# Kernel optimization log

Hardware: AMD Instinct MI355X
Metric: run time of the kernel (lower is better)

The kernel has to match this reference:

```python
import jax, jax.numpy as jnp
import numpy as np

D = 512      # embeddings_dim (in_features == out_features)
H = 4        # num_heads
MID = 2048   # mid_features
B, S = 4, 2048
EPS = 1e-5


def _ln(x, g, b):
    mu = jnp.mean(x, axis=-1, keepdims=True)
    var = jnp.mean(jnp.square(x - mu), axis=-1, keepdims=True)
    return g * (x - mu) / jnp.sqrt(var + EPS) + b


def setup_inputs() -> dict:
    key = jax.random.key(0)
    ks = jax.random.split(key, 16)
    w = 0.02  # weight init scale
    return {
        "x_encoder": jax.random.normal(ks[0], (B, S, D), jnp.float32),
        "x_decoder": jax.random.normal(ks[1], (B, S, D), jnp.float32),
        # per-head full-width projections (each head is a D->D Linear)
        "Wq": jax.random.normal(ks[2], (H, D, D), jnp.float32) * w,
        "bq": jnp.zeros((H, D), jnp.float32),
        "Wk": jax.random.normal(ks[3], (H, D, D), jnp.float32) * w,
        "bk": jnp.zeros((H, D), jnp.float32),
        "Wv": jax.random.normal(ks[4], (H, D, D), jnp.float32) * w,
        "bv": jnp.zeros((H, D), jnp.float32),
        # out_reshaper: Rearrange('b h s d -> b s (d h)') then Linear(D*H -> D)
        "Wo": jax.random.normal(ks[5], (D * H, D), jnp.float32) * w,
        "bo": jnp.zeros((D,), jnp.float32),
        "ln1_g": jnp.ones((D,), jnp.float32), "ln1_b": jnp.zeros((D,), jnp.float32),
        "ln2_g": jnp.ones((D,), jnp.float32), "ln2_b": jnp.zeros((D,), jnp.float32),
        # FouriFeedForward: D -> MID -> D with SELU
        "W1": jax.random.normal(ks[6], (D, MID), jnp.float32) * w,
        "b1": jnp.zeros((MID,), jnp.float32),
        "W2": jax.random.normal(ks[7], (MID, D), jnp.float32) * w,
        "b2": jnp.zeros((D,), jnp.float32),
        "ln3_g": jnp.ones((D,), jnp.float32), "ln3_b": jnp.zeros((D,), jnp.float32),
    }


def reference(x_encoder, x_decoder, Wq, bq, Wk, bk, Wv, bv, Wo, bo,
              ln1_g, ln1_b, ln2_g, ln2_b, W1, b1, W2, b2, ln3_g, ln3_b):
    # Fourier token mixing: per-batch fftn over (seq, feature) dims, keep real part
    xf = jnp.fft.fftn(x_decoder, axes=(1, 2)).real
    xd = _ln(x_decoder + xf, ln1_g, ln1_b)  # [B,S,D]

    # Linear multi-head attention: q from decoder, k/v from encoder.
    # qs/ks/vs: [B,H,S,D]; softmax over the HEAD axis (dim=1 in torch)
    qs = jax.nn.softmax(jnp.einsum('bsd,hde->bhse', xd, Wq) + bq[None, :, None, :], axis=1)
    ks = jax.nn.softmax(jnp.einsum('bsd,hde->bhse', x_encoder, Wk) + bk[None, :, None, :], axis=1)
    vs = jnp.einsum('bsd,hde->bhse', x_encoder, Wv) + bv[None, :, None, :]

    gc = jnp.einsum('bhsd,bhse->bhde', ks, vs)       # [B,H,D,D] global contexts
    out = jnp.einsum('bhsd,bhde->bhse', qs, gc)      # [B,H,S,D]

    # Rearrange 'b h s d -> b s (d h)': d is the slow axis, h the fast axis
    b, h, s, d = out.shape
    out = out.transpose(0, 2, 3, 1).reshape(b, s, d * h)
    attn = out @ Wo + bo                              # [B,S,D]

    x = _ln(xd + attn, ln2_g, ln2_b)
    ff = jax.nn.selu(x @ W1 + b1) @ W2 + b2           # dropout_p=0 (eval)
    x = _ln(x + ff, ln3_g, ln3_b)
    return x
```

## Files before the change

### kernel.cpp

```cpp
#include <hip/hip_runtime.h>
#include <stdint.h>

typedef __bf16 bf16;
typedef __bf16 bf16x8 __attribute__((ext_vector_type(8)));
typedef float f32x4 __attribute__((ext_vector_type(4)));

static __device__ __forceinline__ void async16(const void* g, void* l) {
  __builtin_amdgcn_global_load_lds(
      (__attribute__((address_space(1))) void*)g,
      (__attribute__((address_space(3))) void*)l, 16, 0, 0);
}

__global__ void __launch_bounds__(256) prep_all(
    const float* __restrict__ xdec, const float* __restrict__ xenc,
    bf16* __restrict__ Ttrig, bf16* __restrict__ Atrig2,
    bf16* __restrict__ xdec_b, bf16* __restrict__ xenc_b,
    const float* __restrict__ Wq, const float* __restrict__ Wk,
    const float* __restrict__ Wv, const float* __restrict__ Wo,
    const float* __restrict__ W1, const float* __restrict__ W2,
    bf16* __restrict__ BtQ, bf16* __restrict__ BtK, bf16* __restrict__ BtV,
    bf16* __restrict__ WoTh, bf16* __restrict__ W1T, bf16* __restrict__ W2T) {
  __shared__ bf16 tile[32][33];
  int id = blockIdx.x;
  if (id < 2048) {
    int idx = id * 256 + threadIdx.x;
    int d = idx & 511, jp = idx >> 9;
    int jj = jp >> 1, p = jp & 1;
    int t = (d * jj) & 511;
    float ang = (float)t * (6.283185307179586f / 512.0f);
    Ttrig[idx] = (bf16)(p ? __sinf(ang) : __cosf(ang));
  } else if (id < 11840) {
    int idx = (id - 2048) * 256 + threadIdx.x;
    int k = idx % 1088;
    int rr = idx / 1088;
    int r = rr % 1152, half = rr / 1152;
    float v = 0.0f;
    int tt = (r * k) & 2047;
    float ang = (float)tt * (6.283185307179586f / 2048.0f);
    if (half == 0) { if (r <= 1024 && k <= 1024) v = __cosf(ang); }
    else           { if (r <= 1023 && k >= 1 && k <= 1023) v = -__sinf(ang); }
    Atrig2[idx] = (bf16)v;
  } else if (id < 28224) {
    int i = (id - 11840) * 256 + threadIdx.x;
    xdec_b[i] = (bf16)xdec[i];
  } else if (id < 44608) {
    int i = (id - 28224) * 256 + threadIdx.x;
    xenc_b[i] = (bf16)xenc[i];
  } else {
    int id2 = id - 44608;
    int kind = id2 >> 10, t = id2 & 1023;
    const float* in; bf16* out; int R, C, rt, ct;
    bool iperm = false, qperm = false, hsel = false; int hh = 0;
    if (kind == 0)      { in = Wq; out = BtQ; R = 2048; C = 512; rt = t >> 4; ct = t & 15; iperm = true; qperm = true; }
    else if (kind == 1) { in = Wk; out = BtK; R = 2048; C = 512; rt = t >> 4; ct = t & 15; iperm = true; }
    else if (kind == 2) { in = Wv; out = BtV; R = 2048; C = 512; rt = t >> 4; ct = t & 15; iperm = true; }
    else if (kind == 3) {
      int zz = t >> 8, tt = t & 255;
      in = Wo; out = WoTh + (long)zz * 262144;
      R = 512; C = 512; rt = tt >> 4; ct = tt & 15; hsel = true; hh = zz;
    }
    else if (kind == 4) { in = W1; out = W1T; R = 512; C = 2048; rt = t >> 6; ct = t & 63; }
    else                { in = W2; out = W2T; R = 2048; C = 512; rt = t >> 4; ct = t & 15; }
    int c0 = ct * 32, r0 = rt * 32;
    int tx = threadIdx.x & 31, ty = threadIdx.x >> 5;
#pragma unroll
    for (int i = 0; i < 32; i += 8) {
      int r = r0 + ty + i;
      int rr = hsel ? (4 * r + hh) : r;
      tile[ty + i][tx] = (bf16)in[(long)rr * C + (c0 + tx)];
    }
    __syncthreads();
#pragma unroll
    for (int i = 0; i < 32; i += 8) {
      int cc = c0 + ty + i, rr = r0 + tx;
      if (iperm) {
        int e = cc, h = rr >> 9;
        int n = qperm ? ((e & 15) | (h << 4) | ((e >> 4) << 6)) : (4 * e + h);
        out[((long)n << 9) + (rr & 511)] = tile[tx][ty + i];
      } else {
        out[(long)cc * R + rr] = tile[tx][ty + i];
      }
    }
  }
}

__global__ void __launch_bounds__(256) fold_y(const bf16* __restrict__ Yt,
                                              bf16* __restrict__ Yf2) {
  int idx = blockIdx.x * 256 + threadIdx.x;
  int k = idx % 1088;
  int rr = idx / 1088;
  int j = rr & 511, z = rr >> 9;
  int b = z & 3, half = z >> 2;
  const bf16* yin = Yt + (long)b * 2097152 + (long)j * 4096;
  float v = 0.0f;
  if (half == 0) {
    if (k == 0) v = (float)yin[0];
    else if (k == 1024) v = (float)yin[1024];
    else if (k < 1024) v = (float)yin[k] + (float)yin[2048 - k];
  } else {
    if (k >= 1 && k <= 1023) v = (float)yin[2048 + k] - (float)yin[4096 - k];
  }
  Yf2[(long)z * 557056 + (long)j * 1088 + k] = (bf16)v;
}

__global__ void __launch_bounds__(256) ln1_kernel(
    const float* __restrict__ xdec, const bf16* __restrict__ CSb,
    const float* __restrict__ g, const float* __restrict__ be,
    bf16* __restrict__ outb) {
  const int row = blockIdx.x, t = threadIdx.x;
  const int b = row >> 11, s = row & 2047;
  const int sp = (s <= 1024) ? s : 2048 - s;
  const float sgn = (s <= 1024) ? 1.0f : -1.0f;
  const bf16* Crow = CSb + ((long)b * 1152 + sp) * 512;
  const bf16* Srow = CSb + ((long)(b + 4) * 1152 + sp) * 512;
  const long base = (long)row * 512;
  float v0 = xdec[base + t] + (float)Crow[t] + sgn * (float)Srow[t];
  float v1 = xdec[base + t + 256] + (float)Crow[t + 256] + sgn * (float)Srow[t + 256];
  float sm = v0 + v1, q = v0 * v0 + v1 * v1;
#pragma unroll
  for (int off = 32; off > 0; off >>= 1) {
    sm += __shfl_down(sm, off);
    q += __shfl_down(q, off);
  }
  __shared__ float red[8];
  const int wv = t >> 6, ln = t & 63;
  if (ln == 0) { red[wv] = sm; red[wv + 4] = q; }
  __syncthreads();
  float S = red[0] + red[1] + red[2] + red[3];
  float Q = red[4] + red[5] + red[6] + red[7];
  float mu = S * (1.0f / 512.0f);
  float var = Q * (1.0f / 512.0f) - mu * mu;
  float rstd = rsqrtf(var + 1e-5f);
  outb[base + t] = (bf16)(g[t] * (v0 - mu) * rstd + be[t]);
  outb[base + t + 256] = (bf16)(g[t + 256] * (v1 - mu) * rstd + be[t + 256]);
}

static __device__ __forceinline__ void smkv_body(
    int bid, bf16* lds,
    const bf16* __restrict__ klog, bf16* __restrict__ ksT,
    const bf16* __restrict__ vlog, bf16* __restrict__ vsT) {
  const int t = threadIdx.x;
  const bool isK = bid < 1024;
  int tb = isK ? bid : (bid - 1024);
  const bf16* src = isK ? klog : vlog;
  bf16* dst = isK ? ksT : vsT;
  int b = tb >> 8, rem = tb & 255;
  int s0 = (rem >> 3) << 6, e0 = (rem & 7) << 6;
  int te = t & 63, tr = t >> 6;
#pragma unroll
  for (int i = 0; i < 16; ++i) {
    int s = tr + (i << 2);
    bf16 raw[4] __attribute__((aligned(8)));
    *(uint2*)raw = *(const uint2*)(src + ((long)(b * 2048 + s0 + s) * 2048 + 4 * (e0 + te)));
    float x0 = (float)raw[0], x1 = (float)raw[1], x2 = (float)raw[2], x3 = (float)raw[3];
    if (isK) {
      float m = fmaxf(fmaxf(x0, x1), fmaxf(x2, x3));
      float y0 = __expf(x0 - m), y1 = __expf(x1 - m), y2 = __expf(x2 - m), y3 = __expf(x3 - m);
      float rs = 1.0f / (y0 + y1 + y2 + y3);
      x0 = y0 * rs; x1 = y1 * rs; x2 = y2 * rs; x3 = y3 * rs;
    }
    int cp = ((((s >> 2) ^ (te & 15)) << 2) | (s & 3));
    int base = te * 64 + cp;
    lds[base] = (bf16)x0;
    lds[4096 + base] = (bf16)x1;
    lds[8192 + base] = (bf16)x2;
    lds[12288 + base] = (bf16)x3;
  }
  __syncthreads();
  int sc = t & 15, r = t >> 4;
#pragma unroll
  for (int i = 0; i < 16; ++i) {
    int he = r + (i << 4);
    int h = he >> 6, e = he & 63;
    int cp = (sc ^ (e & 15)) << 2;
    bf16 tmp[4] __attribute__((aligned(8)));
    *(uint2*)tmp = *(const uint2*)&lds[h * 4096 + e * 64 + cp];
    *(uint2*)(dst + ((long)(b * 4 + h) * 512 + e0 + e) * 2048 + s0 + (sc << 2)) =
        *(const uint2*)tmp;
  }
}

template <typename TA, typename TB, int WRITE_BF16, int WRITE_F32>
__global__ void __launch_bounds__(256) ln_kernel(
    const TA* __restrict__ A, const TB* __restrict__ Bv,
    const float* __restrict__ g, const float* __restrict__ be,
    bf16* __restrict__ outb, float* __restrict__ outf) {
  const int row = blockIdx.x, t = threadIdx.x;
  const long base = (long)row * 512;
  float v0 = (float)A[base + t] + (float)Bv[base + t];
  float v1 = (float)A[base + t + 256] + (float)Bv[base + t + 256];
  float s = v0 + v1, q = v0 * v0 + v1 * v1;
#pragma unroll
  for (int off = 32; off > 0; off >>= 1) {
    s += __shfl_down(s, off);
    q += __shfl_down(q, off);
  }
  __shared__ float red[8];
  const int wv = t >> 6, ln = t & 63;
  if (ln == 0) { red[wv] = s; red[wv + 4] = q; }
  __syncthreads();
  float S = red[0] + red[1] + red[2] + red[3];
  float Q = red[4] + red[5] + red[6] + red[7];
  float mu = S * (1.0f / 512.0f);
  float var = Q * (1.0f / 512.0f) - mu * mu;
  float rstd = rsqrtf(var + 1e-5f);
  float o0 = g[t] * (v0 - mu) * rstd + be[t];
  float o1 = g[t + 256] * (v1 - mu) * rstd + be[t + 256];
  if (WRITE_BF16) { outb[base + t] = (bf16)o0; outb[base + t + 256] = (bf16)o1; }
  if (WRITE_F32)  { outf[base + t] = o0; outf[base + t + 256] = o1; }
}

template <int BN, int ADDR_MODE, int HAS_BIAS, int DO_SELU, int F32OUT, int SWIZ,
          int AHEAD>
static __device__ __forceinline__ void gemm_bt_body(
    int id, bf16* lA, bf16* lB,
    const bf16* __restrict__ A, const bf16* __restrict__ Bt,
    const float* __restrict__ bias, void* __restrict__ Cout,
    int N, int K, long sAz, long sBz, long sBiasz, long sCz,
    int gx, int gy, int gin) {
  int x, y, z;
  {
    if (SWIZ == 0) {
      x = id % gx; int t2 = id / gx; y = t2 % gy; z = t2 / gy;
    } else {
      int xcd = id & 7, r = id >> 3;
      int inner = r % gin, G = xcd + 8 * (r / gin);
      if (SWIZ == 1)      { y = G; x = inner % gx; z = inner / gx; }
      else if (SWIZ == 2) { z = G; x = inner % gx; y = inner / gx; }
      else                { x = G; y = inner % gy; z = inner / gy; }
    }
  }
  A  += (AHEAD == 1) ? sAz * (z & 3) : (AHEAD == 2) ? sAz * (z >> 2) : sAz * z;
  Bt += sBz * z;
  const int m0 = y * 128, n0 = x * BN;
  const int t = threadIdx.x;
  const int lane = t & 63, wave = t >> 6;
  const int srow = t >> 3;
  const int pch  = t & 7;
  const int lch  = pch ^ (srow & 7);
  const bf16* Ag = A  + (long)(m0 + srow) * K + lch * 8;
  const bf16* Bg = Bt + (long)(n0 + srow) * K + lch * 8;
  bf16* lAp = lA + srow * 64 + pch * 8;
  bf16* lBp = lB + srow * 64 + pch * 8;
  constexpr int MI = (BN == 128) ? 4 : 2;
  const int wm = (BN == 128) ? (wave >> 1) * 64 : wave * 32;
  const int wn = (BN == 128) ? (wave & 1) * 64 : 0;
  const int fr = lane & 15, fq = lane >> 4;

  f32x4 acc[MI][4] = {};

  for (int k0 = 0; k0 < K; k0 += 64) {
    __syncthreads();
#pragma unroll
    for (int i = 0; i < 4; ++i)
      async16(Ag + k0 + (long)(32 * i) * K, lAp + 32 * i * 64);
#pragma unroll
    for (int i = 0; i < BN / 32; ++i)
      async16(Bg + k0 + (long)(32 * i) * K, lBp + 32 * i * 64);
    __syncthreads();
#pragma unroll
    for (int kk = 0; kk < 2; ++kk) {
      bf16x8 av[MI], bfrag[4];
#pragma unroll
      for (int mi = 0; mi < MI; ++mi) {
        int r = wm + mi * 16 + fr;
        int c = (kk * 4 + fq) ^ (r & 7);
        av[mi] = *(const bf16x8*)&lA[r * 64 + c * 8];
      }
#pragma unroll
      for (int ni = 0; ni < 4; ++ni) {
        int r = wn + ni * 16 + fr;
        int c = (kk * 4 + fq) ^ (r & 7);
        bfrag[ni] = *(const bf16x8*)&lB[r * 64 + c * 8];
      }
#pragma unroll
      for (int mi = 0; mi < MI; ++mi)
#pragma unroll
        for (int ni = 0; ni < 4; ++ni)
          acc[mi][ni] = __builtin_amdgcn_mfma_f32_16x16x32_bf16(
              av[mi], bfrag[ni], acc[mi][ni], 0, 0, 0);
    }
  }

#pragma unroll
  for (int mi = 0; mi < MI; ++mi) {
#pragma unroll
    for (int ni = 0; ni < 4; ++ni) {
      const int col = n0 + wn + ni * 16 + fr;
      float bias_v = 0.0f;
      if (HAS_BIAS == 1) bias_v = bias[sBiasz * z + col];
      if (ADDR_MODE == 7) {
        const int b = z >> 2, h = z & 3;
#pragma unroll
        for (int r = 0; r < 4; ++r) {
          const int row = m0 + wm + mi * 16 + fq * 4 + r;
          ((bf16*)Cout)[((long)(b * 512 + row)) * 2048 + h * 512 + col] =
              (bf16)(acc[mi][ni][r] + bias_v);
        }
      } else if (ADDR_MODE == 9) {
        const int b = z >> 2, h = z & 3;
        const int kidx = (col & 15) | (h << 4) | ((col >> 4) << 6);
#pragma unroll
        for (int r = 0; r < 4; ++r) {
          const int row = m0 + wm + mi * 16 + fq * 4 + r;
          ((bf16*)Cout)[((long)(b * 512 + row)) * 2048 + kidx] =
              (bf16)(acc[mi][ni][r] + bias_v);
        }
      } else {
#pragma unroll
        for (int r = 0; r < 4; ++r) {
          const int row = m0 + wm + mi * 16 + fq * 4 + r;
          float v = acc[mi][ni][r] + bias_v;
          if (DO_SELU) v = v > 0.0f ? 1.0507009873554805f * v
                                    : 1.7580993408473766f * (__expf(v) - 1.0f);
          long addr = sCz * z + (long)row * N + col;
          if (F32OUT) ((float*)Cout)[addr] = v;
          else        ((bf16*)Cout)[addr] = (bf16)v;
        }
      }
    }
  }
}

template <int BN, int ADDR_MODE, int HAS_BIAS, int DO_SELU, int F32OUT, int SWIZ,
          int AHEAD = 0>
__global__ void __launch_bounds__(256, 2) gemm_bt(
    const bf16* __restrict__ A, const bf16* __restrict__ Bt,
    const float* __restrict__ bias, void* __restrict__ Cout,
    int N, int K, long sAz, long sBz, long sBiasz, long sCz,
    int gx, int gy, int gin) {
  __shared__ __align__(16) bf16 lA[128 * 64];
  __shared__ __align__(16) bf16 lB[BN * 64];
  gemm_bt_body<BN, ADDR_MODE, HAS_BIAS, DO_SELU, F32OUT, SWIZ, AHEAD>(
      blockIdx.x, lA, lB, A, Bt, bias, Cout, N, K, sAz, sBz, sBiasz, sCz, gx, gy, gin);
}

static __device__ __forceinline__ void qkv_body(
    int id, bf16* lA, bf16* lB,
    const bf16* __restrict__ Aq, const bf16* __restrict__ Aenc,
    const bf16* __restrict__ BQ, const bf16* __restrict__ BK,
    const bf16* __restrict__ BV,
    const float* __restrict__ bq, const float* __restrict__ bk,
    const float* __restrict__ bv,
    bf16* __restrict__ qs2, bf16* __restrict__ klog, bf16* __restrict__ vlog) {
  const int seg = id >> 10, sid = id & 1023;
  const int xcd = sid & 7, r = sid >> 3;
  const int x = r & 15, y = xcd + 8 * (r >> 4);
  const bf16 *A, *Bt; bf16* out; const float* bias;
  if (seg == 0)      { A = Aq;   Bt = BQ; out = qs2;  bias = bq; }
  else if (seg == 1) { A = Aenc; Bt = BK; out = klog; bias = bk; }
  else               { A = Aenc; Bt = BV; out = vlog; bias = bv; }
  const int K = 512;
  const int m0 = y * 128, n0 = x * 128;
  const int t = threadIdx.x;
  const int lane = t & 63, wave = t >> 6;
  const int srow = t >> 3, pch = t & 7, lch = pch ^ (srow & 7);
  const bf16* Ag = A  + (long)(m0 + srow) * K + lch * 8;
  const bf16* Bg = Bt + (long)(n0 + srow) * K + lch * 8;
  bf16* lAp = lA + srow * 64 + pch * 8;
  bf16* lBp = lB + srow * 64 + pch * 8;
  const int wm = (wave >> 1) * 64, wn = (wave & 1) * 64;
  const int fr = lane & 15, fq = lane >> 4;

  f32x4 acc[4][4] = {};
  for (int k0 = 0; k0 < K; k0 += 64) {
    __syncthreads();
#pragma unroll
    for (int i = 0; i < 4; ++i) {
      async16(Ag + k0 + (long)(32 * i) * K, lAp + 32 * i * 64);
      async16(Bg + k0 + (long)(32 * i) * K, lBp + 32 * i * 64);
    }
    __syncthreads();
#pragma unroll
    for (int kk = 0; kk < 2; ++kk) {
      bf16x8 av[4], bfrag[4];
#pragma unroll
      for (int mi = 0; mi < 4; ++mi) {
        int rr = wm + mi * 16 + fr;
        int c = (kk * 4 + fq) ^ (rr & 7);
        av[mi] = *(const bf16x8*)&lA[rr * 64 + c * 8];
      }
#pragma unroll
      for (int ni = 0; ni < 4; ++ni) {
        int rr = wn + ni * 16 + fr;
        int c = (kk * 4 + fq) ^ (rr & 7);
        bfrag[ni] = *(const bf16x8*)&lB[rr * 64 + c * 8];
      }
#pragma unroll
      for (int mi = 0; mi < 4; ++mi)
#pragma unroll
        for (int ni = 0; ni < 4; ++ni)
          acc[mi][ni] = __builtin_amdgcn_mfma_f32_16x16x32_bf16(
              av[mi], bfrag[ni], acc[mi][ni], 0, 0, 0);
    }
  }

  if (seg == 0) {
    const int ebase = fr + 16 * ((n0 + wn) >> 6);
    const float b0 = bias[ebase], b1 = bias[512 + ebase],
                b2 = bias[1024 + ebase], b3 = bias[1536 + ebase];
#pragma unroll
    for (int mi = 0; mi < 4; ++mi) {
#pragma unroll
      for (int r = 0; r < 4; ++r) {
        const int row = m0 + wm + mi * 16 + fq * 4 + r;
        float v0 = acc[mi][0][r] + b0;
        float v1 = acc[mi][1][r] + b1;
        float v2 = acc[mi][2][r] + b2;
        float v3 = acc[mi][3][r] + b3;
        float m = fmaxf(fmaxf(v0, v1), fmaxf(v2, v3));
        float p0 = __expf(v0 - m), p1 = __expf(v1 - m),
              p2 = __expf(v2 - m), p3 = __expf(v3 - m);
        float rs = 1.0f / (p0 + p1 + p2 + p3);
        const long ob = (long)row * 2048 + n0 + wn + fr;
        out[ob]      = (bf16)(p0 * rs);
        out[ob + 16] = (bf16)(p1 * rs);
        out[ob + 32] = (bf16)(p2 * rs);
        out[ob + 48] = (bf16)(p3 * rs);
      }
    }
  } else {
#pragma unroll
    for (int mi = 0; mi < 4; ++mi) {
#pragma unroll
      for (int ni = 0; ni < 4; ++ni) {
        const int col = n0 + wn + ni * 16 + fr;
        const float bias_v = bias[(col & 3) * 512 + (col >> 2)];
#pragma unroll
        for (int r = 0; r < 4; ++r) {
          const int row = m0 + wm + mi * 16 + fq * 4 + r;
          out[(long)row * 2048 + col] = (bf16)(acc[mi][ni][r] + bias_v);
        }
      }
    }
  }
}

__global__ void __launch_bounds__(256, 2) fused_kv_yt(
    const bf16* __restrict__ Aenc, const bf16* __restrict__ BK,
    const bf16* __restrict__ BV,
    const float* __restrict__ bk, const float* __restrict__ bv,
    bf16* __restrict__ klog, bf16* __restrict__ vlog,
    const bf16* __restrict__ Ttrig, const bf16* __restrict__ xdec_b,
    bf16* __restrict__ Yt) {
  __shared__ __align__(16) bf16 smem[16384];
  int id = blockIdx.x;
  if (id < 2048)
    qkv_body(id + 1024, smem, smem + 8192, nullptr, Aenc, nullptr, BK, BV,
             nullptr, bk, bv, nullptr, klog, vlog);
  else
    gemm_bt_body<128, 0, 0, 0, 0, 3, 0>(id - 2048, smem, smem + 8192,
        Ttrig, xdec_b, nullptr, Yt, 2048, 512, 0L, 1048576L, 0L, 2097152L, 16, 8, 32);
}

__global__ void __launch_bounds__(256, 2) fused_cs_smkv(
    const bf16* __restrict__ klog, bf16* __restrict__ ksT,
    const bf16* __restrict__ vlog, bf16* __restrict__ vsT,
    const bf16* __restrict__ Atrig2, const bf16* __restrict__ Yf2,
    bf16* __restrict__ CSb) {
  __shared__ __align__(16) bf16 smem[16384];
  int id = blockIdx.x;
  if (id < 2048)
    smkv_body(id, smem, klog, ksT, vlog, vsT);
  else
    gemm_bt_body<64, 0, 0, 0, 0, 2, 2>(id - 2048, smem, smem + 8192,
        Atrig2, Yf2, nullptr, CSb, 512, 1088, 1253376L, 557056L, 0L, 589824L, 8, 9, 72);
}

__global__ void __launch_bounds__(256, 2) fused_q_gc(
    const bf16* __restrict__ Aq, const bf16* __restrict__ BQ,
    const float* __restrict__ bq, bf16* __restrict__ qs2,
    const bf16* __restrict__ ksT, const bf16* __restrict__ vsT,
    bf16* __restrict__ gc) {
  __shared__ __align__(16) bf16 smem[16384];
  int id = blockIdx.x;
  if (id < 1024)
    qkv_body(id, smem, smem + 8192, Aq, nullptr, BQ, nullptr, nullptr,
             bq, nullptr, nullptr, qs2, nullptr, nullptr);
  else
    gemm_bt_body<64, 0, 0, 0, 0, 2, 0>(id - 1024, smem, smem + 8192,
        ksT, vsT, nullptr, gc, 512, 2048, 1048576L, 1048576L, 0L, 262144L, 8, 4, 32);
}

extern "C" void kernel_launch(void* const* d_in, const int* in_sizes, int n_in,
                              void* d_out, int out_size, void* d_ws, size_t ws_size,
                              hipStream_t stream) {
  (void)in_sizes; (void)n_in; (void)out_size; (void)ws_size;
  const float* x_enc = (const float*)d_in[0];
  const float* x_dec = (const float*)d_in[1];
  const float* Wq = (const float*)d_in[2];
  const float* bq = (const float*)d_in[3];
  const float* Wk = (const float*)d_in[4];
  const float* bk = (const float*)d_in[5];
  const float* Wv = (const float*)d_in[6];
  const float* bv = (const float*)d_in[7];
  const float* Wo = (const float*)d_in[8];
  const float* bo = (const float*)d_in[9];
  const float* g1 = (const float*)d_in[10];
  const float* be1 = (const float*)d_in[11];
  const float* g2 = (const float*)d_in[12];
  const float* be2 = (const float*)d_in[13];
  const float* W1 = (const float*)d_in[14];
  const float* b1 = (const float*)d_in[15];
  const float* W2 = (const float*)d_in[16];
  const float* b2 = (const float*)d_in[17];
  const float* g3 = (const float*)d_in[18];
  const float* be3 = (const float*)d_in[19];

  char* ws = (char*)d_ws;
  const size_t MB = 1u << 20;
  bf16*  BtQ    = (bf16*) (ws + 0);
  bf16*  midb   = (bf16*) (ws + 0);
  bf16*  klog   = (bf16*) (ws + 32 * MB);
  bf16*  attn_b = (bf16*) (ws + 32 * MB);
  bf16*  vlog   = (bf16*) (ws + 64 * MB);
  bf16*  gc     = (bf16*) (ws + 64 * MB);
  bf16*  ff_b   = (bf16*) (ws + 72 * MB);
  bf16*  Atrig2 = (bf16*) (ws + 96 * MB);
  bf16*  Ttrig  = (bf16*) (ws + 101 * MB);
  bf16*  CSb    = (bf16*) (ws + 102 * MB);
  bf16*  qs2    = (bf16*) (ws + 96 * MB);
  bf16*  xenc_b = (bf16*) (ws + 128 * MB);
  bf16*  BtK    = (bf16*) (ws + 136 * MB);
  bf16*  BtV    = (bf16*) (ws + 138 * MB);
  bf16*  ksT    = (bf16*) (ws + 128 * MB);
  bf16*  vsT    = (bf16*) (ws + 160 * MB);
  bf16*  xd_b   = (bf16*) (ws + 192 * MB);
  bf16*  x2_b   = (bf16*) (ws + 200 * MB);
  bf16*  gwT    = (bf16*) (ws + 208 * MB);
  bf16*  Yt     = (bf16*) (ws + 216 * MB);
  bf16*  Yf2    = (bf16*) (ws + 232 * MB);
  bf16*  WoTh   = (bf16*) (ws + 241 * MB);
  bf16*  W1T    = (bf16*) (ws + 243 * MB);
  bf16*  W2T    = (bf16*) (ws + 245 * MB);
  bf16*  xdec_b = (bf16*) (ws + 247 * MB);

  prep_all<<<50752, 256, 0, stream>>>(x_dec, x_enc, Ttrig, Atrig2, xdec_b, xenc_b,
                                      Wq, Wk, Wv, Wo, W1, W2,
                                      BtQ, BtK, BtV, WoTh, W1T, W2T);

  fused_kv_yt<<<2560, 256, 0, stream>>>(xenc_b, BtK, BtV, bk, bv, klog, vlog,
                                        Ttrig, xdec_b, Yt);

  fold_y<<<17408, 256, 0, stream>>>(Yt, Yf2);

  fused_cs_smkv<<<2624, 256, 0, stream>>>(klog, ksT, vlog, vsT, Atrig2, Yf2, CSb);

  ln1_kernel<<<8192, 256, 0, stream>>>(x_dec, CSb, g1, be1, xd_b);

  fused_q_gc<<<1536, 256, 0, stream>>>(xd_b, BtQ, bq, qs2, ksT, vsT, gc);

  gemm_bt<64, 9, 0, 0, 0, 2, 1><<<512, 256, 0, stream>>>(
      WoTh, gc, nullptr, gwT, 512, 512, 262144L, 262144L, 0L, 0L, 8, 4, 32);
  gemm_bt<64, 0, 1, 0, 0, 1><<<512, 256, 0, stream>>>(
      qs2, gwT, bo, attn_b, 512, 2048, 4194304L, 1048576L, 0L, 1048576L, 8, 16, 32);
  ln_kernel<bf16, bf16, 1, 0><<<8192, 256, 0, stream>>>(
      xd_b, attn_b, g2, be2, x2_b, nullptr);

  gemm_bt<128, 0, 1, 1, 0, 1><<<1024, 256, 0, stream>>>(
      x2_b, W1T, b1, midb, 2048, 512, 0L, 0L, 0L, 0L, 16, 64, 16);
  gemm_bt<64, 0, 1, 0, 0, 1><<<512, 256, 0, stream>>>(
      midb, W2T, b2, ff_b, 512, 2048, 0L, 0L, 0L, 0L, 8, 64, 8);
  ln_kernel<bf16, bf16, 0, 1><<<8192, 256, 0, stream>>>(
      x2_b, ff_b, g3, be3, nullptr, (float*)d_out);
}
```

Before: 410.7 us.

## Fuse K softmax and transpose into KV GEMM epilogue; reschedule gc and gw stages

The K/V projection epilogue now applies the head-axis softmax for K and writes directly in transposed [b,h,e,s] layout. This removes the separate smkv pass that re-read klog/vlog and wrote ksT/vsT. Because of that, the global-context GEMM moves earlier into the same launch as the Fourier CS GEMM, and the Wo·gc GEMM is merged with the Q projection, which drops one kernel launch. The K/V weights are also permuted with the Q-style head interleave so that each thread holds all 4 heads for the epilogue softmax. The trade-off is strided 8-byte stores from the GEMM epilogue and a different workspace aliasing.

New measurement: 381.9 us. 1.08x faster.

```diff
diff --git a/kernel.cpp b/kernel.cpp
--- a/kernel.cpp
+++ b/kernel.cpp
@@ -50,8 +50,8 @@
     int id2 = id - 44608;
     int kind = id2 >> 10, t = id2 & 1023;
     const float* in; bf16* out; int R, C, rt, ct;
-    bool iperm = false, qperm = false, hsel = false; int hh = 0;
-    if (kind == 0)      { in = Wq; out = BtQ; R = 2048; C = 512; rt = t >> 4; ct = t & 15; iperm = true; qperm = true; }
+    bool iperm = false, hsel = false; int hh = 0;
+    if (kind == 0)      { in = Wq; out = BtQ; R = 2048; C = 512; rt = t >> 4; ct = t & 15; iperm = true; }
     else if (kind == 1) { in = Wk; out = BtK; R = 2048; C = 512; rt = t >> 4; ct = t & 15; iperm = true; }
     else if (kind == 2) { in = Wv; out = BtV; R = 2048; C = 512; rt = t >> 4; ct = t & 15; iperm = true; }
     else if (kind == 3) {
@@ -75,7 +75,7 @@
       int cc = c0 + ty + i, rr = r0 + tx;
       if (iperm) {
         int e = cc, h = rr >> 9;
-        int n = qperm ? ((e & 15) | (h << 4) | ((e >> 4) << 6)) : (4 * e + h);
+        int n = (e & 15) | (h << 4) | ((e >> 4) << 6);
         out[((long)n << 9) + (rr & 511)] = tile[tx][ty + i];
       } else {
         out[(long)cc * R + rr] = tile[tx][ty + i];
@@ -133,51 +133,6 @@
   float rstd = rsqrtf(var + 1e-5f);
   outb[base + t] = (bf16)(g[t] * (v0 - mu) * rstd + be[t]);
   outb[base + t + 256] = (bf16)(g[t + 256] * (v1 - mu) * rstd + be[t + 256]);
-}
-
-static __device__ __forceinline__ void smkv_body(
-    int bid, bf16* lds,
-    const bf16* __restrict__ klog, bf16* __restrict__ ksT,
-    const bf16* __restrict__ vlog, bf16* __restrict__ vsT) {
-  const int t = threadIdx.x;
-  const bool isK = bid < 1024;
-  int tb = isK ? bid : (bid - 1024);
-  const bf16* src = isK ? klog : vlog;
-  bf16* dst = isK ? ksT : vsT;
-  int b = tb >> 8, rem = tb & 255;
-  int s0 = (rem >> 3) << 6, e0 = (rem & 7) << 6;
-  int te = t & 63, tr = t >> 6;
-#pragma unroll
-  for (int i = 0; i < 16; ++i) {
-    int s = tr + (i << 2);
-    bf16 raw[4] __attribute__((aligned(8)));
-    *(uint2*)raw = *(const uint2*)(src + ((long)(b * 2048 + s0 + s) * 2048 + 4 * (e0 + te)));
-    float x0 = (float)raw[0], x1 = (float)raw[1], x2 = (float)raw[2], x3 = (float)raw[3];
-    if (isK) {
-      float m = fmaxf(fmaxf(x0, x1), fmaxf(x2, x3));
-      float y0 = __expf(x0 - m), y1 = __expf(x1 - m), y2 = __expf(x2 - m), y3 = __expf(x3 - m);
-      float rs = 1.0f / (y0 + y1 + y2 + y3);
-      x0 = y0 * rs; x1 = y1 * rs; x2 = y2 * rs; x3 = y3 * rs;
-    }
-    int cp = ((((s >> 2) ^ (te & 15)) << 2) | (s & 3));
-    int base = te * 64 + cp;
-    lds[base] = (bf16)x0;
-    lds[4096 + base] = (bf16)x1;
-    lds[8192 + base] = (bf16)x2;
-    lds[12288 + base] = (bf16)x3;
-  }
-  __syncthreads();
-  int sc = t & 15, r = t >> 4;
-#pragma unroll
-  for (int i = 0; i < 16; ++i) {
-    int he = r + (i << 4);
-    int h = he >> 6, e = he & 63;
-    int cp = (sc ^ (e & 15)) << 2;
-    bf16 tmp[4] __attribute__((aligned(8)));
-    *(uint2*)tmp = *(const uint2*)&lds[h * 4096 + e * 64 + cp];
-    *(uint2*)(dst + ((long)(b * 4 + h) * 512 + e0 + e) * 2048 + s0 + (sc << 2)) =
-        *(const uint2*)tmp;
-  }
 }
 
 template <typename TA, typename TB, int WRITE_BF16, int WRITE_F32>
@@ -289,15 +244,7 @@
       const int col = n0 + wn + ni * 16 + fr;
       float bias_v = 0.0f;
       if (HAS_BIAS == 1) bias_v = bias[sBiasz * z + col];
-      if (ADDR_MODE == 7) {
-        const int b = z >> 2, h = z & 3;
-#pragma unroll
-        for (int r = 0; r < 4; ++r) {
-          const int row = m0 + wm + mi * 16 + fq * 4 + r;
-          ((bf16*)Cout)[((long)(b * 512 + row)) * 2048 + h * 512 + col] =
-              (bf16)(acc[mi][ni][r] + bias_v);
-        }
-      } else if (ADDR_MODE == 9) {
+      if (ADDR_MODE == 9) {
         const int b = z >> 2, h = z & 3;
         const int kidx = (col & 15) | (h << 4) | ((col >> 4) << 6);
 #pragma unroll
@@ -342,14 +289,14 @@
     const bf16* __restrict__ BV,
     const float* __restrict__ bq, const float* __restrict__ bk,
     const float* __restrict__ bv,
-    bf16* __restrict__ qs2, bf16* __restrict__ klog, bf16* __restrict__ vlog) {
+    bf16* __restrict__ qs2, bf16* __restrict__ ksT, bf16* __restrict__ vsT) {
   const int seg = id >> 10, sid = id & 1023;
   const int xcd = sid & 7, r = sid >> 3;
   const int x = r & 15, y = xcd + 8 * (r >> 4);
   const bf16 *A, *Bt; bf16* out; const float* bias;
-  if (seg == 0)      { A = Aq;   Bt = BQ; out = qs2;  bias = bq; }
-  else if (seg == 1) { A = Aenc; Bt = BK; out = klog; bias = bk; }
-  else               { A = Aenc; Bt = BV; out = vlog; bias = bv; }
+  if (seg == 0)      { A = Aq;   Bt = BQ; out = qs2; bias = bq; }
+  else if (seg == 1) { A = Aenc; Bt = BK; out = ksT; bias = bk; }
+  else               { A = Aenc; Bt = BV; out = vsT; bias = bv; }
   const int K = 512;
   const int m0 = y * 128, n0 = x * 128;
   const int t = threadIdx.x;
@@ -395,10 +342,10 @@
     }
   }
 
+  const int ebase = fr + 16 * ((n0 + wn) >> 6);
+  const float b0 = bias[ebase], b1 = bias[512 + ebase],
+              b2 = bias[1024 + ebase], b3 = bias[1536 + ebase];
   if (seg == 0) {
-    const int ebase = fr + 16 * ((n0 + wn) >> 6);
-    const float b0 = bias[ebase], b1 = bias[512 + ebase],
-                b2 = bias[1024 + ebase], b3 = bias[1536 + ebase];
 #pragma unroll
     for (int mi = 0; mi < 4; ++mi) {
 #pragma unroll
@@ -420,18 +367,31 @@
       }
     }
   } else {
+    const int bb = m0 >> 11;
 #pragma unroll
     for (int mi = 0; mi < 4; ++mi) {
-#pragma unroll
-      for (int ni = 0; ni < 4; ++ni) {
-        const int col = n0 + wn + ni * 16 + fr;
-        const float bias_v = bias[(col & 3) * 512 + (col >> 2)];
-#pragma unroll
-        for (int r = 0; r < 4; ++r) {
-          const int row = m0 + wm + mi * 16 + fq * 4 + r;
-          out[(long)row * 2048 + col] = (bf16)(acc[mi][ni][r] + bias_v);
+      const int s_base = (m0 & 2047) + wm + mi * 16 + fq * 4;
+      bf16 tmp[4][4] __attribute__((aligned(8)));
+#pragma unroll
+      for (int r = 0; r < 4; ++r) {
+        float v0 = acc[mi][0][r] + b0;
+        float v1 = acc[mi][1][r] + b1;
+        float v2 = acc[mi][2][r] + b2;
+        float v3 = acc[mi][3][r] + b3;
+        if (seg == 1) {
+          float m = fmaxf(fmaxf(v0, v1), fmaxf(v2, v3));
+          float p0 = __expf(v0 - m), p1 = __expf(v1 - m),
+                p2 = __expf(v2 - m), p3 = __expf(v3 - m);
+          float rs = 1.0f / (p0 + p1 + p2 + p3);
+          v0 = p0 * rs; v1 = p1 * rs; v2 = p2 * rs; v3 = p3 * rs;
         }
-      }
+        tmp[0][r] = (bf16)v0; tmp[1][r] = (bf16)v1;
+        tmp[2][r] = (bf16)v2; tmp[3][r] = (bf16)v3;
+      }
+#pragma unroll
+      for (int ni = 0; ni < 4; ++ni)
+        *(uint2*)(out + ((long)((bb * 4 + ni) * 512 + ebase)) * 2048 + s_base) =
+            *(const uint2*)tmp[ni];
     }
   }
 }
@@ -440,46 +400,47 @@
     const bf16* __restrict__ Aenc, const bf16* __restrict__ BK,
     const bf16* __restrict__ BV,
     const float* __restrict__ bk, const float* __restrict__ bv,
-    bf16* __restrict__ klog, bf16* __restrict__ vlog,
+    bf16* __restrict__ ksT, bf16* __restrict__ vsT,
     const bf16* __restrict__ Ttrig, const bf16* __restrict__ xdec_b,
     bf16* __restrict__ Yt) {
   __shared__ __align__(16) bf16 smem[16384];
   int id = blockIdx.x;
   if (id < 2048)
     qkv_body(id + 1024, smem, smem + 8192, nullptr, Aenc, nullptr, BK, BV,
-             nullptr, bk, bv, nullptr, klog, vlog);
+             nullptr, bk, bv, nullptr, ksT, vsT);
   else
     gemm_bt_body<128, 0, 0, 0, 0, 3, 0>(id - 2048, smem, smem + 8192,
         Ttrig, xdec_b, nullptr, Yt, 2048, 512, 0L, 1048576L, 0L, 2097152L, 16, 8, 32);
 }
 
-__global__ void __launch_bounds__(256, 2) fused_cs_smkv(
-    const bf16* __restrict__ klog, bf16* __restrict__ ksT,
-    const bf16* __restrict__ vlog, bf16* __restrict__ vsT,
+__global__ void __launch_bounds__(256, 2) fused_gc_cs(
+    const bf16* __restrict__ ksT, const bf16* __restrict__ vsT,
+    bf16* __restrict__ gc,
     const bf16* __restrict__ Atrig2, const bf16* __restrict__ Yf2,
     bf16* __restrict__ CSb) {
-  __shared__ __align__(16) bf16 smem[16384];
+  __shared__ __align__(16) bf16 smem[12288];
   int id = blockIdx.x;
-  if (id < 2048)
-    smkv_body(id, smem, klog, ksT, vlog, vsT);
+  if (id < 512)
+    gemm_bt_body<64, 0, 0, 0, 0, 2, 0>(id, smem, smem + 8192,
+        ksT, vsT, nullptr, gc, 512, 2048, 1048576L, 1048576L, 0L, 262144L, 8, 4, 32);
   else
-    gemm_bt_body<64, 0, 0, 0, 0, 2, 2>(id - 2048, smem, smem + 8192,
+    gemm_bt_body<64, 0, 0, 0, 0, 2, 2>(id - 512, smem, smem + 8192,
         Atrig2, Yf2, nullptr, CSb, 512, 1088, 1253376L, 557056L, 0L, 589824L, 8, 9, 72);
 }
 
-__global__ void __launch_bounds__(256, 2) fused_q_gc(
+__global__ void __launch_bounds__(256, 2) fused_q_gw(
     const bf16* __restrict__ Aq, const bf16* __restrict__ BQ,
     const float* __restrict__ bq, bf16* __restrict__ qs2,
-    const bf16* __restrict__ ksT, const bf16* __restrict__ vsT,
-    bf16* __restrict__ gc) {
+    const bf16* __restrict__ WoTh, const bf16* __restrict__ gc,
+    bf16* __restrict__ gwT) {
   __shared__ __align__(16) bf16 smem[16384];
   int id = blockIdx.x;
   if (id < 1024)
     qkv_body(id, smem, smem + 8192, Aq, nullptr, BQ, nullptr, nullptr,
              bq, nullptr, nullptr, qs2, nullptr, nullptr);
   else
-    gemm_bt_body<64, 0, 0, 0, 0, 2, 0>(id - 1024, smem, smem + 8192,
-        ksT, vsT, nullptr, gc, 512, 2048, 1048576L, 1048576L, 0L, 262144L, 8, 4, 32);
+    gemm_bt_body<64, 9, 0, 0, 0, 2, 1>(id - 1024, smem, smem + 8192,
+        WoTh, gc, nullptr, gwT, 512, 512, 262144L, 262144L, 0L, 0L, 8, 4, 32);
 }
 
 extern "C" void kernel_launch(void* const* d_in, const int* in_sizes, int n_in,
@@ -511,10 +472,9 @@
   const size_t MB = 1u << 20;
   bf16*  BtQ    = (bf16*) (ws + 0);
   bf16*  midb   = (bf16*) (ws + 0);
-  bf16*  klog   = (bf16*) (ws + 32 * MB);
+  bf16*  ksT    = (bf16*) (ws + 32 * MB);
   bf16*  attn_b = (bf16*) (ws + 32 * MB);
-  bf16*  vlog   = (bf16*) (ws + 64 * MB);
-  bf16*  gc     = (bf16*) (ws + 64 * MB);
+  bf16*  vsT    = (bf16*) (ws + 64 * MB);
   bf16*  ff_b   = (bf16*) (ws + 72 * MB);
   bf16*  Atrig2 = (bf16*) (ws + 96 * MB);
   bf16*  Ttrig  = (bf16*) (ws + 101 * MB);
@@ -523,12 +483,11 @@
   bf16*  xenc_b = (bf16*) (ws + 128 * MB);
   bf16*  BtK    = (bf16*) (ws + 136 * MB);
   bf16*  BtV    = (bf16*) (ws + 138 * MB);
-  bf16*  ksT    = (bf16*) (ws + 128 * MB);
-  bf16*  vsT    = (bf16*) (ws + 160 * MB);
   bf16*  xd_b   = (bf16*) (ws + 192 * MB);
   bf16*  x2_b   = (bf16*) (ws + 200 * MB);
   bf16*  gwT    = (bf16*) (ws + 208 * MB);
   bf16*  Yt     = (bf16*) (ws + 216 * MB);
+  bf16*  gc     = (bf16*) (ws + 216 * MB);
   bf16*  Yf2    = (bf16*) (ws + 232 * MB);
   bf16*  WoTh   = (bf16*) (ws + 241 * MB);
   bf16*  W1T    = (bf16*) (ws + 243 * MB);
@@ -539,19 +498,17 @@
                                       Wq, Wk, Wv, Wo, W1, W2,
                                       BtQ, BtK, BtV, WoTh, W1T, W2T);
 
-  fused_kv_yt<<<2560, 256, 0, stream>>>(xenc_b, BtK, BtV, bk, bv, klog, vlog,
+  fused_kv_yt<<<2560, 256, 0, stream>>>(xenc_b, BtK, BtV, bk, bv, ksT, vsT,
                                         Ttrig, xdec_b, Yt);
 
   fold_y<<<17408, 256, 0, stream>>>(Yt, Yf2);
 
-  fused_cs_smkv<<<2624, 256, 0, stream>>>(klog, ksT, vlog, vsT, Atrig2, Yf2, CSb);
+  fused_gc_cs<<<1088, 256, 0, stream>>>(ksT, vsT, gc, Atrig2, Yf2, CSb);
 
   ln1_kernel<<<8192, 256, 0, stream>>>(x_dec, CSb, g1, be1, xd_b);
 
-  fused_q_gc<<<1536, 256, 0, stream>>>(xd_b, BtQ, bq, qs2, ksT, vsT, gc);
-
-  gemm_bt<64, 9, 0, 0, 0, 2, 1><<<512, 256, 0, stream>>>(
-      WoTh, gc, nullptr, gwT, 512, 512, 262144L, 262144L, 0L, 0L, 8, 4, 32);
+  fused_q_gw<<<1536, 256, 0, stream>>>(xd_b, BtQ, bq, qs2, WoTh, gc, gwT);
+
   gemm_bt<64, 0, 1, 0, 0, 1><<<512, 256, 0, stream>>>(
       qs2, gwT, bo, attn_b, 512, 2048, 4194304L, 1048576L, 0L, 1048576L, 8, 16, 32);
   ln_kernel<bf16, bf16, 1, 0><<<8192, 256, 0, stream>>>(
```
